# Optimization experiments

Measured on AMD Instinct MI355X. Metric: run time of the kernel, lower is better.

Reference implementation:

```python
import jax, jax.numpy as jnp
import numpy as np

# pywt db4 decomposition filters (dec_lo, dec_hi), 8 taps
DEC_LO = np.array([-0.010597401784997278, 0.032883011666982945, 0.030841381835986965,
                   -0.18703481171888114, -0.02798376941698385, 0.6308807679295904,
                   0.7148465705525415, 0.23037781330885523])
DEC_HI = np.array([-0.23037781330885523, 0.7148465705525415, -0.6308807679295904,
                   -0.02798376941698385, 0.18703481171888114, 0.030841381835986965,
                   -0.032883011666982945, -0.010597401784997278])
HEADS = 8


def dwt_db4(v):
    # Equivalent of pywt.dwt(v, 'db4') (mode='symmetric') applied along last axis.
    # Symmetric (half-point) extension by L-1=7, full convolution, downsample taking
    # every 2nd sample starting at conv index 1 -> out_len = floor((n+7)/2).
    pad = [(0, 0)] * (v.ndim - 1) + [(7, 7)]
    ext = jnp.pad(v, pad, mode='symmetric')[..., 1:]
    lead = v.shape[:-1]
    lhs = ext.reshape(-1, 1, ext.shape[-1])                       # (N, 1, n+13)
    rhs = jnp.stack([jnp.asarray(DEC_LO[::-1], v.dtype),
                     jnp.asarray(DEC_HI[::-1], v.dtype)])[:, None, :]  # (2, 1, 8)
    out = jax.lax.conv_general_dilated(lhs, rhs, (2,), 'VALID')   # (N, 2, out_len)
    out = out.reshape(*lead, 2, -1)
    return out[..., 0, :], out[..., 1, :]


def setup_inputs() -> dict:
    key = jax.random.key(0)
    k0, k1, k2, k3 = jax.random.split(key, 4)
    B, S, H = 4, 2048, 1024
    a = float(np.sqrt(6.0 / (H + H)))  # xavier_uniform bound
    x = jax.random.normal(k0, (B, S, H), dtype=jnp.float32)
    Wq = jax.random.uniform(k1, (H, H), jnp.float32, -a, a)
    Wk = jax.random.uniform(k2, (H, H), jnp.float32, -a, a)
    Wv = jax.random.uniform(k3, (H, H), jnp.float32, -a, a)
    return {"x": x, "Wq": Wq, "Wk": Wk, "Wv": Wv}


def reference(x, Wq, Wk, Wv):
    B, S, Hd = x.shape
    H = HEADS
    dk = Hd // H
    scale = dk ** -0.5
    # torch nn.Linear: y = x @ W.T
    q = (x @ Wq.T).reshape(B, S, H, dk).transpose(0, 2, 1, 3) * scale  # (B,H,S,dk)
    k = (x @ Wk.T).reshape(B, S, H, dk).transpose(0, 2, 1, 3)
    v = (x @ Wv.T).reshape(B, S, H, dk).transpose(0, 2, 1, 3)
    attn = jax.nn.softmax(jnp.einsum('bhqd,bhkd->bhqk', q, k), axis=-1)
    cA, cD = dwt_db4(v)                                   # (B,H,S,wA) each
    wA = cA.shape[-1]
    wcD = jnp.einsum('bhqk,bhkw->bhqw', attn, cD)
    out1 = wcD.transpose(0, 2, 1, 3).reshape(B, S, H * wA)
    out2 = cA.reshape(-1, S, H * wA)                      # faithful raw view of (B,H,S,wA)
    return out1, out2
```

## Files before the change

### kernel.cpp

```cpp
#include <hip/hip_runtime.h>
#include <hip/hip_bf16.h>

#define B_ 4
#define S_ 2048
#define HD 1024
#define NH 8
#define DK 128
#define WA 67
#define WPAD 80
#define NWROWS 640

typedef __attribute__((ext_vector_type(8))) short short8;
typedef __attribute__((ext_vector_type(4))) short short4v;
typedef __attribute__((ext_vector_type(4))) float floatx4;

__device__ __forceinline__ float hexp2(float x) { return __builtin_amdgcn_exp2f(x); }

__device__ __forceinline__ short f2bf(float f) {
    union { float f; unsigned u; } c; c.f = f;
    unsigned u = c.u;
    u += 0x7FFF + ((u >> 16) & 1);
    return (short)(u >> 16);
}
__device__ __forceinline__ float bf2f(short s) {
    union { unsigned u; float f; } c; c.u = ((unsigned)(unsigned short)s) << 16;
    return c.f;
}
__device__ __forceinline__ short f2bf_trunc(float f) {
    union { float f; unsigned u; } c; c.f = f;
    return (short)(c.u >> 16);
}

__device__ __forceinline__ void glds16(void* lds, const void* g) {
    __builtin_amdgcn_global_load_lds(
        (const __attribute__((address_space(1))) unsigned*)g,
        (__attribute__((address_space(3))) unsigned*)lds, 16, 0, 0);
}

__device__ __constant__ float FLO[8] = {
    0.23037781330885523f,  0.7148465705525415f,  0.6308807679295904f,
   -0.02798376941698385f, -0.18703481171888114f, 0.030841381835986965f,
    0.032883011666982945f, -0.010597401784997278f };
__device__ __constant__ float FHI[8] = {
   -0.010597401784997278f, -0.032883011666982945f, 0.030841381835986965f,
    0.18703481171888114f,  -0.02798376941698385f, -0.6308807679295904f,
    0.7148465705525415f,   -0.23037781330885523f };

__global__ __launch_bounds__(256) void prep_all(
    const float* __restrict__ x,  const float* __restrict__ wq,
    const float* __restrict__ wk, const float* __restrict__ wv,
    short* __restrict__ xb, short* __restrict__ wqk,
    short* __restrict__ wa, short* __restrict__ wg, short* __restrict__ cdt)
{
    const size_t w_elems = (size_t)HD * HD;
    int blk = blockIdx.x;
    if (blk < 5120) {
        const float* src; short* dst; int lb;
        if (blk < 4096)      { src = x;  dst = xb;            lb = blk; }
        else if (blk < 4608) { src = wq; dst = wqk;           lb = blk - 4096; }
        else                 { src = wk; dst = wqk + w_elems; lb = blk - 4608; }
        int i = lb * 256 + threadIdx.x;
        const float4* s = (const float4*)src + (size_t)i * 2;
        float4 f0 = s[0], f1 = s[1];
        short8 o;
        o[0] = f2bf(f0.x); o[1] = f2bf(f0.y); o[2] = f2bf(f0.z); o[3] = f2bf(f0.w);
        o[4] = f2bf(f1.x); o[5] = f2bf(f1.y); o[6] = f2bf(f1.z); o[7] = f2bf(f1.w);
        *((short8*)dst + i) = o;
    } else if (blk < 5388) {
        int idx = (blk - 5120) * 256 + threadIdx.x;
        int j  = idx >> 7;
        int c0 = (idx & 127) * 8;
        unsigned h = (unsigned)j / 67u;
        unsigned t = (unsigned)j - h * 67u;
        float aa[8] = {}, gg[8] = {};
        #pragma unroll
        for (int jj = 0; jj < 8; ++jj) {
            int i = 2 * (int)t + jj;
            int k = (i < 6) ? (5 - i) : (i < 134) ? (i - 6) : (261 - i);
            const float4* wr =
                (const float4*)(wv + ((size_t)(h * 128 + k)) * HD + c0);
            float4 v0 = wr[0], v1 = wr[1];
            float fl = FLO[jj], fh = FHI[jj];
            aa[0] += fl * v0.x; aa[1] += fl * v0.y; aa[2] += fl * v0.z; aa[3] += fl * v0.w;
            aa[4] += fl * v1.x; aa[5] += fl * v1.y; aa[6] += fl * v1.z; aa[7] += fl * v1.w;
            gg[0] += fh * v0.x; gg[1] += fh * v0.y; gg[2] += fh * v0.z; gg[3] += fh * v0.w;
            gg[4] += fh * v1.x; gg[5] += fh * v1.y; gg[6] += fh * v1.z; gg[7] += fh * v1.w;
        }
        short8 oa, og;
        #pragma unroll
        for (int q = 0; q < 8; ++q) { oa[q] = f2bf(aa[q]); og[q] = f2bf(gg[q]); }
        *(short8*)&wa[(size_t)j * HD + c0] = oa;
        *(short8*)&wg[(size_t)j * HD + c0] = og;
    } else {
        int idx = (blk - 5388) * 256 + threadIdx.x;
        int within = idx * 8;
        int row = within >> 11;
        int s0  = within & 2047;
        int bh = row / 13, tr = row - bh * 13;
        short val = (tr == 0) ? (short)0x3F80 : (short)0;
        short8 o = { val, val, val, val, val, val, val, val };
        *(short8*)&cdt[((size_t)bh * WPAD + 67 + tr) * S_ + s0] = o;
    }
}

__global__ __launch_bounds__(256) void mega_gemm(
    const short* __restrict__ xb, const short* __restrict__ wqk,
    const short* __restrict__ wa, const short* __restrict__ wg,
    short* __restrict__ Qb, short* __restrict__ Kb,
    float* __restrict__ out2, short* __restrict__ cdt)
{
    __shared__ __align__(16) short As[128 * 64];
    __shared__ __align__(16) short Bs[128 * 64];
    const int tid  = threadIdx.x;
    const int wv   = tid >> 6;
    const int lane = tid & 63;
    const int l15  = lane & 15;
    const int quad = lane >> 4;
    const int m0 = blockIdx.x * 128;
    const int y  = blockIdx.y;
    int z, n0; const short* W;
    if (y < 8)       { z = 0; n0 = y * 128;        W = wqk; }
    else if (y < 16) { z = 1; n0 = (y - 8) * 128;  W = wqk + (size_t)HD * HD; }
    else if (y < 21) { z = 2; n0 = (y - 16) * 128; W = wa; }
    else             { z = 3; n0 = (y - 21) * 128; W = wg; }
    const float scale = (z == 0) ? 0.12751743786072596f : 1.0f;
    const int wm = (wv & 1) * 64;
    const int wn = (wv >> 1) * 64;
    const int srow = lane >> 3;
    const int sch  = (lane & 7) ^ (srow & 7);
    const int rxor = (l15 & 7);

    floatx4 acc[4][4] = {};
    for (int kk = 0; kk < HD; kk += 64) {
        __syncthreads();
        #pragma unroll
        for (int i = 0; i < 4; ++i) {
            int ti = wv * 4 + i;
            int r  = ti * 8 + srow;
            glds16(As + ti * 512, xb + (size_t)(m0 + r) * HD + kk + sch * 8);
            glds16(Bs + ti * 512, W  + (size_t)(n0 + r) * HD + kk + sch * 8);
        }
        __syncthreads();
        #pragma unroll
        for (int s4 = 0; s4 < 2; ++s4) {
            short8 a[4], b[4];
            #pragma unroll
            for (int t = 0; t < 4; ++t) {
                int ch = (s4 * 4 + quad) ^ rxor;
                a[t] = *(const short8*)&As[(wm + t * 16 + l15) * 64 + ch * 8];
                b[t] = *(const short8*)&Bs[(wn + t * 16 + l15) * 64 + ch * 8];
            }
            #pragma unroll
            for (int mt = 0; mt < 4; ++mt)
                #pragma unroll
                for (int nt = 0; nt < 4; ++nt)
                    acc[mt][nt] = __builtin_amdgcn_mfma_f32_16x16x32_bf16(
                        a[mt], b[nt], acc[mt][nt], 0, 0, 0);
        }
    }
    if (z < 2) {
        short* Yb = (z == 0) ? Qb : Kb;
        #pragma unroll
        for (int mt = 0; mt < 4; ++mt)
            #pragma unroll
            for (int nt = 0; nt < 4; ++nt)
                #pragma unroll
                for (int reg = 0; reg < 4; ++reg) {
                    int rg = m0 + wm + mt * 16 + quad * 4 + reg;
                    int cg = n0 + wn + nt * 16 + l15;
                    int b = rg >> 11, s = rg & 2047;
                    int h = cg >> 7,  d = cg & 127;
                    Yb[((size_t)(b * NH + h) * S_ + s) * DK + d] =
                        f2bf(acc[mt][nt][reg] * scale);
                }
    } else {
        #pragma unroll
        for (int mt = 0; mt < 4; ++mt)
            #pragma unroll
            for (int nt = 0; nt < 4; ++nt)
                #pragma unroll
                for (int reg = 0; reg < 4; ++reg) {
                    int rg = m0 + wm + mt * 16 + quad * 4 + reg;
                    int j  = n0 + wn + nt * 16 + l15;
                    if (j < NH * WA) {
                        int b = rg >> 11, s = rg & 2047;
                        unsigned h = (unsigned)j / 67u;
                        unsigned t = (unsigned)j - h * 67u;
                        if (z == 2)
                            out2[((size_t)(b * NH + (int)h) * S_ + s) * WA + t] =
                                acc[mt][nt][reg];
                        else
                            cdt[((size_t)(b * NH + (int)h) * WPAD + t) * S_ + s] =
                                f2bf(acc[mt][nt][reg]);
                    }
                }
    }
}

__global__ __launch_bounds__(256, 2) void attn_kernel(
    const short* __restrict__ Qb, const short* __restrict__ Kb,
    const short* __restrict__ cdt, float* __restrict__ out1)
{
    __shared__ __align__(16) short Ks[64 * 128];
    __shared__ __align__(16) short Ds[WPAD * 64];
    __shared__ __align__(16) short Pt[8 * 1024];
    const int tid  = threadIdx.x;
    const int wv   = tid >> 6;
    const int lane = tid & 63;
    const int l15  = lane & 15;
    const int quad = lane >> 4;
    const int qt = blockIdx.x;
    const int bh = blockIdx.y;
    const int b = bh >> 3, h = bh & 7;
    const int rxor = l15 & 7;

    short8 aq[2][4];
    #pragma unroll
    for (int n = 0; n < 2; ++n) {
        const short* qrow =
            Qb + ((size_t)bh * S_ + qt * 128 + wv * 32 + n * 16 + l15) * DK;
        #pragma unroll
        for (int s4 = 0; s4 < 4; ++s4)
            aq[n][s4] = *(const short8*)(qrow + s4 * 32 + quad * 8);
    }

    floatx4 O[2][5] = {};

    const short* kbase = Kb + (size_t)bh * S_ * DK;
    const int krow = lane >> 4;
    const int kch  = (lane & 15);
    const int drow = lane >> 3;
    const int dch  = (lane & 7) ^ (drow & 7);
    short* ptw = Pt + wv * 2048;

    for (int kt = 0; kt < 32; ++kt) {
        __syncthreads();
        #pragma unroll
        for (int i = 0; i < 4; ++i) {
            int ti = wv * 4 + i;
            int r  = ti * 4 + krow;
            int ch = kch ^ (r & 7);
            glds16(Ks + ti * 512, kbase + ((size_t)kt * 64 + r) * DK + ch * 8);
        }
        #pragma unroll
        for (int i = 0; i < 3; ++i) {
            int t = wv + i * 4;
            if (t < 10) {
                int r = t * 8 + drow;
                glds16(Ds + t * 512,
                       cdt + ((size_t)bh * WPAD + r) * S_ + kt * 64 + dch * 8);
            }
        }
        __syncthreads();

        floatx4 sc[2][4] = {};
        #pragma unroll
        for (int s4 = 0; s4 < 4; ++s4) {
            short8 kf[4];
            #pragma unroll
            for (int mt = 0; mt < 4; ++mt) {
                int ch = (s4 * 4 + quad) ^ rxor;
                kf[mt] = *(const short8*)&Ks[(mt * 16 + l15) * 128 + ch * 8];
            }
            #pragma unroll
            for (int n = 0; n < 2; ++n)
                #pragma unroll
                for (int mt = 0; mt < 4; ++mt)
                    sc[n][mt] = __builtin_amdgcn_mfma_f32_16x16x32_bf16(
                        kf[mt], aq[n][s4], sc[n][mt], 0, 0, 0);
        }
        #pragma unroll
        for (int n = 0; n < 2; ++n) {
            #pragma unroll
            for (int mt = 0; mt < 4; ++mt) {
                short4v pk;
                #pragma unroll
                for (int reg = 0; reg < 4; ++reg)
                    pk[reg] = f2bf_trunc(hexp2(sc[n][mt][reg]));
                int ch = (mt * 2 + (quad >> 1)) ^ rxor;
                *(short4v*)&ptw[n * 1024 + l15 * 64 + ch * 8 + (quad & 1) * 4] = pk;
            }
        }
        short8 ap[2][2];
        #pragma unroll
        for (int mt = 0; mt < 2; ++mt)
            #pragma unroll
            for (int ks = 0; ks < 2; ++ks) {
                int ch = (ks * 4 + quad) ^ rxor;
                ap[mt][ks] = *(const short8*)&ptw[mt * 1024 + l15 * 64 + ch * 8];
            }
        #pragma unroll
        for (int j = 0; j < 5; ++j) {
            #pragma unroll
            for (int ks = 0; ks < 2; ++ks) {
                int ch = (ks * 4 + quad) ^ rxor;
                short8 bd = *(const short8*)&Ds[(j * 16 + l15) * 64 + ch * 8];
                #pragma unroll
                for (int mt = 0; mt < 2; ++mt)
                    O[mt][j] = __builtin_amdgcn_mfma_f32_16x16x32_bf16(
                        ap[mt][ks], bd, O[mt][j], 0, 0, 0);
            }
        }
    }
    float rl[2][4];
    #pragma unroll
    for (int mt = 0; mt < 2; ++mt)
        #pragma unroll
        for (int reg = 0; reg < 4; ++reg)
            rl[mt][reg] = 1.0f / __shfl(O[mt][4][reg], (quad << 4) | 3, 64);
    #pragma unroll
    for (int mt = 0; mt < 2; ++mt)
        #pragma unroll
        for (int j = 0; j < 5; ++j) {
            int w = j * 16 + l15;
            if (w < WA) {
                #pragma unroll
                for (int reg = 0; reg < 4; ++reg) {
                    int qrow_g = qt * 128 + wv * 32 + mt * 16 + quad * 4 + reg;
                    out1[((size_t)(b * S_ + qrow_g)) * (NH * WA) + h * WA + w] =
                        O[mt][j][reg] * rl[mt][reg];
                }
            }
        }
}

extern "C" void kernel_launch(void* const* d_in, const int* in_sizes, int n_in,
                              void* d_out, int out_size, void* d_ws, size_t ws_size,
                              hipStream_t stream)
{
    const float* x  = (const float*)d_in[0];
    const float* Wq = (const float*)d_in[1];
    const float* Wk = (const float*)d_in[2];
    const float* Wv = (const float*)d_in[3];
    float* out = (float*)d_out;

    const size_t x_elems   = (size_t)B_ * S_ * HD;
    const size_t w_elems   = (size_t)HD * HD;
    const size_t qkv_elems = (size_t)B_ * NH * S_ * DK;
    short* xb  = (short*)d_ws;
    short* Wqk = xb + x_elems;
    short* Wa  = Wqk + 2 * w_elems;
    short* Wg  = Wa + (size_t)NWROWS * HD;
    short* Qb  = Wg + (size_t)NWROWS * HD;
    short* Kb  = Qb + qkv_elems;
    short* cdt = Kb + qkv_elems;
    float* out1 = out;
    float* out2 = out + (size_t)B_ * S_ * NH * WA;

    prep_all<<<dim3(5804), 256, 0, stream>>>(x, Wq, Wk, Wv, xb, Wqk, Wa, Wg, cdt);
    mega_gemm<<<dim3(64, 26), 256, 0, stream>>>(xb, Wqk, Wa, Wg, Qb, Kb, out2, cdt);
    attn_kernel<<<dim3(16, 32), 256, 0, stream>>>(Qb, Kb, cdt, out1);
}
```

Measured before the change: 246.9 us.

## Stage wavelet GEMM epilogues through shared memory for coalesced stores

The cA and cD projection epilogues now write accumulators into a padded shared-memory tile, then store to global memory in coalesced order, with vectorized short4 stores for the transposed cD layout. The blockIdx.y mapping is reordered so the wavelet blocks are scheduled first. The out2 path now round-trips through bf16 in shared memory, which loses precision compared with the previous direct fp32 store. The padded tile also enlarges shared memory per block.

```diff
diff --git a/kernel.cpp b/kernel.cpp
--- a/kernel.cpp
+++ b/kernel.cpp
@@ -109,8 +109,10 @@
     short* __restrict__ Qb, short* __restrict__ Kb,
     float* __restrict__ out2, short* __restrict__ cdt)
 {
-    __shared__ __align__(16) short As[128 * 64];
-    __shared__ __align__(16) short Bs[128 * 64];
+    __shared__ __align__(16) short smem[128 * 132];
+    short* As = smem;
+    short* Bs = smem + 128 * 64;
+    short* Cs = smem;
     const int tid  = threadIdx.x;
     const int wv   = tid >> 6;
     const int lane = tid & 63;
@@ -119,10 +121,10 @@
     const int m0 = blockIdx.x * 128;
     const int y  = blockIdx.y;
     int z, n0; const short* W;
-    if (y < 8)       { z = 0; n0 = y * 128;        W = wqk; }
-    else if (y < 16) { z = 1; n0 = (y - 8) * 128;  W = wqk + (size_t)HD * HD; }
-    else if (y < 21) { z = 2; n0 = (y - 16) * 128; W = wa; }
-    else             { z = 3; n0 = (y - 21) * 128; W = wg; }
+    if (y < 5)       { z = 3; n0 = y * 128;        W = wg; }
+    else if (y < 10) { z = 2; n0 = (y - 5) * 128;  W = wa; }
+    else if (y < 18) { z = 0; n0 = (y - 10) * 128; W = wqk; }
+    else             { z = 1; n0 = (y - 18) * 128; W = wqk + (size_t)HD * HD; }
     const float scale = (z == 0) ? 0.12751743786072596f : 1.0f;
     const int wm = (wv & 1) * 64;
     const int wn = (wv >> 1) * 64;
@@ -173,27 +175,55 @@
                     Yb[((size_t)(b * NH + h) * S_ + s) * DK + d] =
                         f2bf(acc[mt][nt][reg] * scale);
                 }
+        return;
+    }
+    __syncthreads();
+    if (z == 3) {
+        #pragma unroll
+        for (int mt = 0; mt < 4; ++mt)
+            #pragma unroll
+            for (int nt = 0; nt < 4; ++nt)
+                #pragma unroll
+                for (int reg = 0; reg < 4; ++reg)
+                    Cs[(wn + nt * 16 + l15) * 132 + wm + mt * 16 + quad * 4 + reg] =
+                        f2bf(acc[mt][nt][reg]);
     } else {
         #pragma unroll
         for (int mt = 0; mt < 4; ++mt)
             #pragma unroll
             for (int nt = 0; nt < 4; ++nt)
                 #pragma unroll
-                for (int reg = 0; reg < 4; ++reg) {
-                    int rg = m0 + wm + mt * 16 + quad * 4 + reg;
-                    int j  = n0 + wn + nt * 16 + l15;
-                    if (j < NH * WA) {
-                        int b = rg >> 11, s = rg & 2047;
-                        unsigned h = (unsigned)j / 67u;
-                        unsigned t = (unsigned)j - h * 67u;
-                        if (z == 2)
-                            out2[((size_t)(b * NH + (int)h) * S_ + s) * WA + t] =
-                                acc[mt][nt][reg];
-                        else
-                            cdt[((size_t)(b * NH + (int)h) * WPAD + t) * S_ + s] =
-                                f2bf(acc[mt][nt][reg]);
-                    }
-                }
+                for (int reg = 0; reg < 4; ++reg)
+                    Cs[(wm + mt * 16 + quad * 4 + reg) * 132 + wn + nt * 16 + l15] =
+                        f2bf(acc[mt][nt][reg]);
+    }
+    __syncthreads();
+    const int b  = m0 >> 11;
+    const int s0 = m0 & 2047;
+    if (z == 3) {
+        for (int c = tid; c < 4096; c += 256) {
+            int jl  = c >> 5;
+            int col = (c & 31) * 4;
+            int j = n0 + jl;
+            if (j < NH * WA) {
+                unsigned h = (unsigned)j / 67u;
+                unsigned t = (unsigned)j - h * 67u;
+                *(short4v*)&cdt[((size_t)(b * NH + (int)h) * WPAD + t) * S_ + s0 + col] =
+                    *(const short4v*)&Cs[jl * 132 + col];
+            }
+        }
+    } else {
+        for (int e = tid; e < 16384; e += 256) {
+            int sl = e >> 7;
+            int jl = e & 127;
+            int j = n0 + jl;
+            if (j < NH * WA) {
+                unsigned h = (unsigned)j / 67u;
+                unsigned t = (unsigned)j - h * 67u;
+                out2[((size_t)(b * NH + (int)h) * S_ + s0 + sl) * WA + t] =
+                    bf2f(Cs[sl * 132 + jl]);
+            }
+        }
     }
 }
 
```

Result: slower. 288.3 us (+16.8%).
